# Optimization experiments

Measured on AMD Instinct MI355X. Metric: run time of the kernel, lower is better.

The kernel has to match this reference:

```python
import jax, jax.numpy as jnp
import numpy as np

N, E, D = 50000, 1200000, 64
NEG_SLOPE = 0.2  # PyG GATConv LeakyReLU slope
EPS_SM = 1e-16   # PyG softmax eps
EPS_LN = 1e-5


def _glorot(key, shape):
    fan = shape[0]
    return jax.random.normal(key, shape, jnp.float32) / np.float32(np.sqrt(fan))


def setup_inputs() -> dict:
    key = jax.random.key(0)
    ks = jax.random.split(key, 16)
    inp = {
        "x": jax.random.normal(ks[0], (N, D), jnp.float32),
        "edge_index": jax.random.randint(ks[1], (2, E), 0, N, dtype=jnp.int32),
        # layer 0: bipartite-style (-1,-1) GATConv -> separate src/dst projections
        "W_src0": _glorot(ks[2], (D, D)), "W_dst0": _glorot(ks[3], (D, D)),
        "a_src0": _glorot(ks[4], (D,)), "a_dst0": _glorot(ks[5], (D,)),
        "b0": jnp.zeros((D,), jnp.float32),
        "lin_W0": _glorot(ks[6], (D, D)), "lin_b0": jnp.zeros((D,), jnp.float32),
        # layers 1,2: int in_channels -> shared projection for src and dst
        "W1": _glorot(ks[7], (D, D)),
        "a_src1": _glorot(ks[8], (D,)), "a_dst1": _glorot(ks[9], (D,)),
        "b1": jnp.zeros((D,), jnp.float32),
        "lin_W1": _glorot(ks[10], (D, D)), "lin_b1": jnp.zeros((D,), jnp.float32),
        "W2": _glorot(ks[11], (D, D)),
        "a_src2": _glorot(ks[12], (D,)), "a_dst2": _glorot(ks[13], (D,)),
        "b2": jnp.zeros((D,), jnp.float32),
        "lin_W2": _glorot(ks[14], (D, D)), "lin_b2": jnp.zeros((D,), jnp.float32),
        "ln_w": jnp.ones((D,), jnp.float32), "ln_b": jnp.zeros((D,), jnp.float32),
        "proj_W": _glorot(ks[15], (D, 1)), "proj_b": jnp.zeros((1,), jnp.float32),
    }
    return inp


def _gat(x_src, x_dst, a_src, a_dst, bias, src, dst):
    # per-edge attention logit: a_src.x_j + a_dst.x_i, LeakyReLU
    alpha = (x_src * a_src).sum(-1)[src] + (x_dst * a_dst).sum(-1)[dst]  # [E]
    alpha = jnp.where(alpha >= 0, alpha, NEG_SLOPE * alpha)
    # segment softmax over edges sharing a destination node
    m = jax.ops.segment_max(alpha, dst, num_segments=N)
    m = jnp.where(jnp.isfinite(m), m, 0.0)  # empty segments -> -inf -> 0
    e = jnp.exp(alpha - m[dst])
    denom = jax.ops.segment_sum(e, dst, num_segments=N)
    w = e / (denom[dst] + EPS_SM)
    # weighted scatter-add aggregation
    return jax.ops.segment_sum(w[:, None] * x_src[src], dst, num_segments=N) + bias


def reference(x, edge_index,
              W_src0, W_dst0, a_src0, a_dst0, b0, lin_W0, lin_b0,
              W1, a_src1, a_dst1, b1, lin_W1, lin_b1,
              W2, a_src2, a_dst2, b2, lin_W2, lin_b2,
              ln_w, ln_b, proj_W, proj_b):
    src, dst = edge_index[0], edge_index[1]
    h = _gat(x @ W_src0, x @ W_dst0, a_src0, a_dst0, b0, src, dst) + x @ lin_W0 + lin_b0
    h = jax.nn.relu(h)
    hp = h @ W1
    h = _gat(hp, hp, a_src1, a_dst1, b1, src, dst) + h @ lin_W1 + lin_b1
    h = jax.nn.relu(h)
    hp = h @ W2
    h = _gat(hp, hp, a_src2, a_dst2, b2, src, dst) + h @ lin_W2 + lin_b2
    # PyG LayerNorm mode='graph': normalize over all nodes and channels
    mu = h.mean()
    var = h.var()
    h = (h - mu) * jax.lax.rsqrt(var + EPS_LN) * ln_w + ln_b
    return h @ proj_W + proj_b  # [N, 1]
```

## Files before the change

kernel.cpp:

```cpp
#include <hip/hip_runtime.h>
#include <hip/hip_bf16.h>

#define NN 50000
#define NE 1200000
#define D 64
#define NEG_SLOPE 0.2f
#define EPS_SM 1e-16f
#define EPS_LN 1e-5f
#define KMAX 4
#define BSH 6
#define NBUK 782
#define BCAP 2048
#define BCAPSH 11
#define EPB 4096
#define NPB 293
#define GP_NODES 32
#define GP_BLOCKS 1563
#define GAT_BLOCKS 12500

__device__ __forceinline__ float waveReduceSum(float v) {
    #pragma unroll
    for (int off = 32; off > 0; off >>= 1)
        v += __shfl_xor(v, off, 64);
    return v;
}
__device__ __forceinline__ float waveReduceMax(float v) {
    #pragma unroll
    for (int off = 32; off > 0; off >>= 1)
        v = fmaxf(v, __shfl_xor(v, off, 64));
    return v;
}
__device__ __forceinline__ float bflo(unsigned v) { return __uint_as_float(v << 16); }
__device__ __forceinline__ float bfhi(unsigned v) { return __uint_as_float(v & 0xffff0000u); }

template <bool HASD>
__global__ __launch_bounds__(256) void gemm_proj(
                          const float* __restrict__ hin,
                          const float* __restrict__ Wsrc,
                          const float* __restrict__ Wdst,
                          const float* __restrict__ Wlin,
                          const float* __restrict__ avs,
                          const float* __restrict__ avd,
                          const float* __restrict__ bgat,
                          const float* __restrict__ blin,
                          __hip_bfloat16* __restrict__ hp,
                          float* __restrict__ agg,
                          float* __restrict__ alpha_s,
                          float* __restrict__ alpha_d) {
    __shared__ float xt[GP_NODES * D];
    const int t   = threadIdx.x;
    const int nb0 = blockIdx.x * GP_NODES;
    const float4* src4 = (const float4*)(hin + (size_t)nb0 * D);
    float4* dst4 = (float4*)xt;
    if (nb0 + GP_NODES <= NN) {
        dst4[t]       = src4[t];
        dst4[t + 256] = src4[t + 256];
    } else {
        #pragma unroll
        for (int i = 0; i < 2; ++i) {
            const int idx = t + 256 * i;
            const int node = nb0 + (idx >> 4);
            dst4[idx] = (node < NN) ? src4[idx] : make_float4(0.f, 0.f, 0.f, 0.f);
        }
    }
    __syncthreads();

    const int wv   = t >> 6;
    const int lane = t & 63;
    const float* xw = xt + wv * 8 * D;

    float accs[8], accl[8], accd[HASD ? 8 : 1];
    #pragma unroll
    for (int m = 0; m < 8; ++m) { accs[m] = 0.f; accl[m] = 0.f; }
    if (HASD) {
        #pragma unroll
        for (int m = 0; m < 8; ++m) accd[m] = 0.f;
    }

    #pragma unroll 4
    for (int k = 0; k < D; k += 4) {
        float ws[4], wl[4], wd[4];
        #pragma unroll
        for (int j = 0; j < 4; ++j) {
            ws[j] = Wsrc[(k + j) * D + lane];
            wl[j] = Wlin[(k + j) * D + lane];
            if (HASD) wd[j] = Wdst[(k + j) * D + lane];
        }
        #pragma unroll
        for (int m = 0; m < 8; ++m) {
            const float4 xm = *(const float4*)(xw + m * D + k);
            accs[m] = fmaf(xm.x, ws[0], accs[m]);
            accs[m] = fmaf(xm.y, ws[1], accs[m]);
            accs[m] = fmaf(xm.z, ws[2], accs[m]);
            accs[m] = fmaf(xm.w, ws[3], accs[m]);
            accl[m] = fmaf(xm.x, wl[0], accl[m]);
            accl[m] = fmaf(xm.y, wl[1], accl[m]);
            accl[m] = fmaf(xm.z, wl[2], accl[m]);
            accl[m] = fmaf(xm.w, wl[3], accl[m]);
            if (HASD) {
                accd[m] = fmaf(xm.x, wd[0], accd[m]);
                accd[m] = fmaf(xm.y, wd[1], accd[m]);
                accd[m] = fmaf(xm.z, wd[2], accd[m]);
                accd[m] = fmaf(xm.w, wd[3], accd[m]);
            }
        }
    }

    const float avs_l = avs[lane], avd_l = avd[lane];
    const float bias  = blin[lane] + bgat[lane];
    #pragma unroll
    for (int m = 0; m < 8; ++m) {
        const int node = nb0 + wv * 8 + m;
        const float vs = waveReduceSum(accs[m] * avs_l);
        const float vd = waveReduceSum((HASD ? accd[m] : accs[m]) * avd_l);
        if (node < NN) {
            hp[(size_t)node * D + lane]  = __float2bfloat16(accs[m]);
            agg[(size_t)node * D + lane] = accl[m] + bias;
            if (lane == 0) {
                alpha_s[node] = vs;
                alpha_d[node] = vd;
            }
        }
    }
}

__global__ __launch_bounds__(256) void bucket_partition(const int* __restrict__ ei,
                                                        int* __restrict__ bcur,
                                                        int2* __restrict__ pairs) {
    __shared__ int h[NBUK];
    __shared__ int cur[NBUK];
    for (int i = threadIdx.x; i < NBUK; i += 256) h[i] = 0;
    __syncthreads();
    const int base = blockIdx.x * EPB;
    const int lim  = min(EPB, NE - base);
    for (int i = threadIdx.x; i < lim; i += 256)
        atomicAdd(&h[ei[NE + base + i] >> BSH], 1);
    __syncthreads();
    for (int i = threadIdx.x; i < NBUK; i += 256) {
        const int c = h[i];
        cur[i] = c ? atomicAdd(&bcur[i], c) : 0;
    }
    __syncthreads();
    for (int i = threadIdx.x; i < lim; i += 256) {
        const int s = ei[base + i];
        const int d = ei[NE + base + i];
        const int b = d >> BSH;
        const int pos = atomicAdd(&cur[b], 1);
        if (pos < BCAP) pairs[(b << BCAPSH) + pos] = make_int2(s, d);
    }
}

__global__ __launch_bounds__(256) void csr_finalize(const int2* __restrict__ pairs,
                                                    const int* __restrict__ bcur,
                                                    int* __restrict__ cnt,
                                                    int* __restrict__ row_start,
                                                    int* __restrict__ csr_src) {
    __shared__ int ncnt[64];
    __shared__ int lsrc[BCAP];
    const int t = threadIdx.x;
    const int b = blockIdx.x;
    const int beg = b << BCAPSH;
    const int m = min(bcur[b], BCAP);
    const int nbase = b << BSH;
    if (t < 64) ncnt[t] = 0;
    __syncthreads();
    for (int i = t; i < m; i += 256)
        atomicAdd(&ncnt[pairs[beg + i].y - nbase], 1);
    __syncthreads();
    if (t < 64) {
        const int v = ncnt[t];
        int inc = v;
        #pragma unroll
        for (int off = 1; off < 64; off <<= 1) {
            const int u = __shfl_up(inc, off, 64);
            if (t >= off) inc += u;
        }
        const int excl = inc - v;
        if (nbase + t < NN) {
            cnt[nbase + t] = v;
            row_start[nbase + t] = beg + excl;
        }
        ncnt[t] = excl;
    }
    __syncthreads();
    for (int i = t; i < m; i += 256) {
        const int2 p = pairs[beg + i];
        const int pos = atomicAdd(&ncnt[p.y - nbase], 1);
        lsrc[pos] = p.x;
    }
    __syncthreads();
    for (int i = t; i < m; i += 256)
        csr_src[beg + i] = lsrc[i];
}

template <bool DO_RELU, bool DO_STATS>
__global__ __launch_bounds__(256) void gat_node(
                         const int* __restrict__ csr_src,
                         const int* __restrict__ row_start,
                         const int* __restrict__ cnt,
                         const float* __restrict__ as,
                         const float* __restrict__ ad,
                         const __hip_bfloat16* __restrict__ hp,
                         float* __restrict__ agg,
                         float* __restrict__ partial) {
    __shared__ int2 esm[4][KMAX * 64];
    const int wv   = threadIdx.x >> 6;
    const int lane = threadIdx.x & 63;
    const int node = blockIdx.x * 4 + wv;
    const int snode = __builtin_amdgcn_readfirstlane(node);
    const int deg = cnt[snode];
    const int rs  = row_start[snode];
    const int half = lane >> 5;
    const int c2   = lane & 31;
    float2 acc = make_float2(0.f, 0.f);
    if (deg > 0) {
        const float ad_d = ad[snode];
        int   sr[KMAX];
        float ea[KMAX];
        float mx = -INFINITY;
        #pragma unroll
        for (int k = 0; k < KMAX; ++k) {
            const int j = k * 64 + lane;
            const bool valid = j < deg;
            const int s = valid ? csr_src[rs + j] : 0;
            float a = valid ? (as[s] + ad_d) : -INFINITY;
            a = (a >= 0.f) ? a : NEG_SLOPE * a;
            sr[k] = s;
            ea[k] = a;
            mx = fmaxf(mx, a);
        }
        mx = waveReduceMax(mx);
        float sum = 0.f;
        #pragma unroll
        for (int k = 0; k < KMAX; ++k) {
            float e = __expf(ea[k] - mx);
            e = (k * 64 + lane < deg) ? e : 0.f;
            ea[k] = e;
            sum += e;
        }
        sum = waveReduceSum(sum);
        const float inv = 1.f / (sum + EPS_SM);
        #pragma unroll
        for (int k = 0; k < KMAX; ++k) {
            if (k * 64 < deg)
                esm[wv][k * 64 + lane] = make_int2(sr[k] * 32, __float_as_int(ea[k] * inv));
        }
        const unsigned* hp32 = (const unsigned*)hp;
        const int jmax = (deg + 1) & ~1;
        float2 a0 = make_float2(0.f, 0.f), a1 = make_float2(0.f, 0.f);
        int j = 0;
        for (; j + 16 <= jmax; j += 16) {
            int2 p[8];
            unsigned v[8];
            #pragma unroll
            for (int u = 0; u < 8; ++u) p[u] = esm[wv][j + 2 * u + half];
            #pragma unroll
            for (int u = 0; u < 8; ++u) v[u] = hp32[p[u].x + c2];
            #pragma unroll
            for (int u = 0; u < 8; ++u) {
                const float w = __int_as_float(p[u].y);
                if (u & 1) {
                    a1.x = fmaf(w, bflo(v[u]), a1.x);
                    a1.y = fmaf(w, bfhi(v[u]), a1.y);
                } else {
                    a0.x = fmaf(w, bflo(v[u]), a0.x);
                    a0.y = fmaf(w, bfhi(v[u]), a0.y);
                }
            }
        }
        for (; j + 4 <= jmax; j += 4) {
            const int2 p0 = esm[wv][j + 0 + half];
            const int2 p1 = esm[wv][j + 2 + half];
            const unsigned v0 = hp32[p0.x + c2];
            const unsigned v1 = hp32[p1.x + c2];
            const float w0 = __int_as_float(p0.y), w1 = __int_as_float(p1.y);
            a0.x = fmaf(w0, bflo(v0), a0.x);
            a0.y = fmaf(w0, bfhi(v0), a0.y);
            a1.x = fmaf(w1, bflo(v1), a1.x);
            a1.y = fmaf(w1, bfhi(v1), a1.y);
        }
        for (; j < jmax; j += 2) {
            const int2 p = esm[wv][j + half];
            const unsigned v = hp32[p.x + c2];
            const float w = __int_as_float(p.y);
            a0.x = fmaf(w, bflo(v), a0.x);
            a0.y = fmaf(w, bfhi(v), a0.y);
        }
        acc.x = a0.x + a1.x;
        acc.y = a0.y + a1.y;
    }
    acc.x += __shfl_xor(acc.x, 32, 64);
    acc.y += __shfl_xor(acc.y, 32, 64);

    float2 r2 = make_float2(0.f, 0.f);
    if (half == 0) {
        const float2 g = *(const float2*)(agg + (size_t)node * D + 2 * c2);
        r2.x = g.x + acc.x;
        r2.y = g.y + acc.y;
        if (DO_RELU) { r2.x = fmaxf(r2.x, 0.f); r2.y = fmaxf(r2.y, 0.f); }
        *(float2*)(agg + (size_t)node * D + 2 * c2) = r2;
    }
    if (DO_STATS) {
        float s  = r2.x + r2.y;
        float ss = r2.x * r2.x + r2.y * r2.y;
        s  = waveReduceSum(s);
        ss = waveReduceSum(ss);
        __shared__ float red[2][4];
        if (lane == 0) { red[0][wv] = s; red[1][wv] = ss; }
        __syncthreads();
        if (threadIdx.x == 0) {
            partial[blockIdx.x]              = red[0][0] + red[0][1] + red[0][2] + red[0][3];
            partial[GAT_BLOCKS + blockIdx.x] = red[1][0] + red[1][1] + red[1][2] + red[1][3];
        }
    }
}

__global__ void ln_reduce(const float* __restrict__ partial, float* __restrict__ stats) {
    float s = 0.f, ss = 0.f;
    for (int i = threadIdx.x; i < GAT_BLOCKS; i += 256) {
        s  += partial[i];
        ss += partial[GAT_BLOCKS + i];
    }
    s  = waveReduceSum(s);
    ss = waveReduceSum(ss);
    __shared__ float sm[2][4];
    if ((threadIdx.x & 63) == 0) {
        sm[0][threadIdx.x >> 6] = s;
        sm[1][threadIdx.x >> 6] = ss;
    }
    __syncthreads();
    if (threadIdx.x == 0) {
        stats[0] = sm[0][0] + sm[0][1] + sm[0][2] + sm[0][3];
        stats[1] = sm[1][0] + sm[1][1] + sm[1][2] + sm[1][3];
    }
}

__global__ void finalize(const float* __restrict__ x,
                         const float* __restrict__ stats,
                         const float* __restrict__ lnw,
                         const float* __restrict__ lnb,
                         const float* __restrict__ pw,
                         const float* __restrict__ pb,
                         float* __restrict__ out) {
    const int wave = (blockIdx.x * blockDim.x + threadIdx.x) >> 6;
    const int lane = threadIdx.x & 63;
    if (wave >= NN) return;
    const float inv_nd = 1.f / (float)(NN * D);
    const float mu  = stats[0] * inv_nd;
    const float var = stats[1] * inv_nd - mu * mu;
    const float rs = rsqrtf(var + EPS_LN);
    const float v = x[(size_t)wave * D + lane];
    const float xn = (v - mu) * rs * lnw[lane] + lnb[lane];
    const float c = waveReduceSum(xn * pw[lane]);
    if (lane == 0) out[wave] = c + pb[0];
}

extern "C" void kernel_launch(void* const* d_in, const int* in_sizes, int n_in,
                              void* d_out, int out_size, void* d_ws, size_t ws_size,
                              hipStream_t stream) {
    const float* x     = (const float*)d_in[0];
    const int*   ei    = (const int*)d_in[1];
    const float* Wsrc0 = (const float*)d_in[2];
    const float* Wdst0 = (const float*)d_in[3];
    const float* asrc0 = (const float*)d_in[4];
    const float* adst0 = (const float*)d_in[5];
    const float* b0    = (const float*)d_in[6];
    const float* linW0 = (const float*)d_in[7];
    const float* linb0 = (const float*)d_in[8];
    const float* W1    = (const float*)d_in[9];
    const float* asrc1 = (const float*)d_in[10];
    const float* adst1 = (const float*)d_in[11];
    const float* b1    = (const float*)d_in[12];
    const float* linW1 = (const float*)d_in[13];
    const float* linb1 = (const float*)d_in[14];
    const float* W2    = (const float*)d_in[15];
    const float* asrc2 = (const float*)d_in[16];
    const float* adst2 = (const float*)d_in[17];
    const float* b2    = (const float*)d_in[18];
    const float* linW2 = (const float*)d_in[19];
    const float* linb2 = (const float*)d_in[20];
    const float* lnw   = (const float*)d_in[21];
    const float* lnb   = (const float*)d_in[22];
    const float* pW    = (const float*)d_in[23];
    const float* pb    = (const float*)d_in[24];
    float* out = (float*)d_out;

    int*  csr_src   = (int*)d_ws;
    int*  cnt       = csr_src + NBUK * BCAP;
    int*  row_start = cnt + NN;
    int*  bcur      = row_start + NN;
    size_t off = (size_t)(NBUK * BCAP + 2 * NN + NBUK);
    off = (off + 3) & ~(size_t)3;
    float* A     = (float*)d_ws + off;
    int2*  pairs = (int2*)A;
    float* B     = A + (size_t)NBUK * BCAP * 2;
    __hip_bfloat16* P = (__hip_bfloat16*)(B + NN * D);
    float* alpha_s = (float*)(P + NN * D);
    float* alpha_d = alpha_s + NN;
    float* stats   = alpha_d + NN;
    float* partial = stats + 2;

    const int elem_blocks = (NN * D) / 256;

    hipMemsetAsync(bcur, 0, NBUK * sizeof(int), stream);
    bucket_partition<<<NPB, 256, 0, stream>>>(ei, bcur, pairs);
    csr_finalize<<<NBUK, 256, 0, stream>>>(pairs, bcur, cnt, row_start, csr_src);

    gemm_proj<true><<<GP_BLOCKS, 256, 0, stream>>>(x, Wsrc0, Wdst0, linW0, asrc0, adst0,
                                                   b0, linb0, P, A, alpha_s, alpha_d);
    gat_node<true, false><<<GAT_BLOCKS, 256, 0, stream>>>(csr_src, row_start, cnt,
                                                          alpha_s, alpha_d, P, A, partial);

    gemm_proj<false><<<GP_BLOCKS, 256, 0, stream>>>(A, W1, W1, linW1, asrc1, adst1,
                                                    b1, linb1, P, B, alpha_s, alpha_d);
    gat_node<true, false><<<GAT_BLOCKS, 256, 0, stream>>>(csr_src, row_start, cnt,
                                                          alpha_s, alpha_d, P, B, partial);

    gemm_proj<false><<<GP_BLOCKS, 256, 0, stream>>>(B, W2, W2, linW2, asrc2, adst2,
                                                    b2, linb2, P, A, alpha_s, alpha_d);
    gat_node<false, true><<<GAT_BLOCKS, 256, 0, stream>>>(csr_src, row_start, cnt,
                                                          alpha_s, alpha_d, P, A, partial);

    ln_reduce<<<1, 256, 0, stream>>>(partial, stats);
    finalize<<<elem_blocks, 256, 0, stream>>>(A, stats, lnw, lnb, pW, pb, out);
}
```

Baseline: 362.8 us.

## Split GAT into softmax pass and channel-group-partitioned aggregation over feature slices

The fused per-node GAT kernel is split into a softmax kernel that writes normalized edge weights to a buffer, and an aggregation kernel launched four times as many blocks, each handling one 16-channel group. Projected features are stored in a group-major bf16 layout so each group's gather touches a 32-byte slice per source, with 8 edges processed per wave iteration. This aims to shrink the gathered working set per pass for better cache hit rates and more parallelism. In exchange it adds an extra kernel, a round trip of edge weights through memory, repeated CSR reads per group, and a much larger partial-sum array for the final reduction.

```diff
diff --git a/kernel.cpp b/kernel.cpp
--- a/kernel.cpp
+++ b/kernel.cpp
@@ -17,6 +17,8 @@
 #define GP_NODES 32
 #define GP_BLOCKS 1563
 #define GAT_BLOCKS 12500
+#define AGG_BLOCKS 50000
+#define NPART 50000
 
 __device__ __forceinline__ float waveReduceSum(float v) {
     #pragma unroll
@@ -43,7 +45,7 @@
                           const float* __restrict__ avd,
                           const float* __restrict__ bgat,
                           const float* __restrict__ blin,
-                          __hip_bfloat16* __restrict__ hp,
+                          unsigned* __restrict__ hpt,
                           float* __restrict__ agg,
                           float* __restrict__ alpha_s,
                           float* __restrict__ alpha_d) {
@@ -108,13 +110,22 @@
 
     const float avs_l = avs[lane], avd_l = avd[lane];
     const float bias  = blin[lane] + bgat[lane];
+    const int grp = lane >> 4;
+    const int cwi = (lane & 15) >> 1;
     #pragma unroll
     for (int m = 0; m < 8; ++m) {
         const int node = nb0 + wv * 8 + m;
         const float vs = waveReduceSum(accs[m] * avs_l);
         const float vd = waveReduceSum((HASD ? accd[m] : accs[m]) * avd_l);
+        __hip_bfloat16 hb = __float2bfloat16(accs[m]);
+        unsigned short raw;
+        __builtin_memcpy(&raw, &hb, 2);
+        const unsigned nbr = (unsigned)__shfl_down((int)raw, 1, 64) & 0xffffu;
         if (node < NN) {
-            hp[(size_t)node * D + lane]  = __float2bfloat16(accs[m]);
+            if (!(lane & 1)) {
+                const unsigned packed = (unsigned)raw | (nbr << 16);
+                hpt[(size_t)grp * (NN * 8) + (size_t)node * 8 + cwi] = packed;
+            }
             agg[(size_t)node * D + lane] = accl[m] + bias;
             if (lane == 0) {
                 alpha_s[node] = vs;
@@ -193,95 +204,100 @@
         csr_src[beg + i] = lsrc[i];
 }
 
-template <bool DO_RELU, bool DO_STATS>
-__global__ __launch_bounds__(256) void gat_node(
+__global__ __launch_bounds__(256) void gat_softmax(
                          const int* __restrict__ csr_src,
                          const int* __restrict__ row_start,
                          const int* __restrict__ cnt,
                          const float* __restrict__ as,
                          const float* __restrict__ ad,
-                         const __hip_bfloat16* __restrict__ hp,
-                         float* __restrict__ agg,
-                         float* __restrict__ partial) {
-    __shared__ int2 esm[4][KMAX * 64];
+                         float* __restrict__ wbuf) {
     const int wv   = threadIdx.x >> 6;
     const int lane = threadIdx.x & 63;
     const int node = blockIdx.x * 4 + wv;
     const int snode = __builtin_amdgcn_readfirstlane(node);
     const int deg = cnt[snode];
+    if (deg <= 0) return;
     const int rs  = row_start[snode];
-    const int half = lane >> 5;
-    const int c2   = lane & 31;
+    const float ad_d = ad[snode];
+    float ea[KMAX];
+    float mx = -INFINITY;
+    #pragma unroll
+    for (int k = 0; k < KMAX; ++k) {
+        const int j = k * 64 + lane;
+        const bool valid = j < deg;
+        const int s = valid ? csr_src[rs + j] : 0;
+        float a = valid ? (as[s] + ad_d) : -INFINITY;
+        a = (a >= 0.f) ? a : NEG_SLOPE * a;
+        ea[k] = a;
+        mx = fmaxf(mx, a);
+    }
+    mx = waveReduceMax(mx);
+    float sum = 0.f;
+    #pragma unroll
+    for (int k = 0; k < KMAX; ++k) {
+        float e = __expf(ea[k] - mx);
+        e = (k * 64 + lane < deg) ? e : 0.f;
+        ea[k] = e;
+        sum += e;
+    }
+    sum = waveReduceSum(sum);
+    const float inv = 1.f / (sum + EPS_SM);
+    #pragma unroll
+    for (int k = 0; k < KMAX; ++k) {
+        const int j = k * 64 + lane;
+        if (j < deg) wbuf[rs + j] = ea[k] * inv;
+    }
+}
+
+template <bool DO_RELU, bool DO_STATS>
+__global__ __launch_bounds__(256) void gat_agg(
+                         const int* __restrict__ csr_src,
+                         const int* __restrict__ row_start,
+                         const int* __restrict__ cnt,
+                         const float* __restrict__ wbuf,
+                         const unsigned* __restrict__ hpt,
+                         float* __restrict__ agg,
+                         float* __restrict__ partial) {
+    __shared__ int2 esm[4][KMAX * 64];
+    const int wv    = threadIdx.x >> 6;
+    const int lane  = threadIdx.x & 63;
+    const int group = blockIdx.x & 3;
+    const int node  = (blockIdx.x >> 2) * 4 + wv;
+    const int snode = __builtin_amdgcn_readfirstlane(node);
+    const int deg = cnt[snode];
+    const int rs  = row_start[snode];
+    const unsigned* gbase = hpt + (size_t)(blockIdx.x & 3) * (NN * 8);
     float2 acc = make_float2(0.f, 0.f);
     if (deg > 0) {
-        const float ad_d = ad[snode];
-        int   sr[KMAX];
-        float ea[KMAX];
-        float mx = -INFINITY;
         #pragma unroll
         for (int k = 0; k < KMAX; ++k) {
-            const int j = k * 64 + lane;
-            const bool valid = j < deg;
-            const int s = valid ? csr_src[rs + j] : 0;
-            float a = valid ? (as[s] + ad_d) : -INFINITY;
-            a = (a >= 0.f) ? a : NEG_SLOPE * a;
-            sr[k] = s;
-            ea[k] = a;
-            mx = fmaxf(mx, a);
-        }
-        mx = waveReduceMax(mx);
-        float sum = 0.f;
-        #pragma unroll
-        for (int k = 0; k < KMAX; ++k) {
-            float e = __expf(ea[k] - mx);
-            e = (k * 64 + lane < deg) ? e : 0.f;
-            ea[k] = e;
-            sum += e;
-        }
-        sum = waveReduceSum(sum);
-        const float inv = 1.f / (sum + EPS_SM);
-        #pragma unroll
-        for (int k = 0; k < KMAX; ++k) {
-            if (k * 64 < deg)
-                esm[wv][k * 64 + lane] = make_int2(sr[k] * 32, __float_as_int(ea[k] * inv));
-        }
-        const unsigned* hp32 = (const unsigned*)hp;
-        const int jmax = (deg + 1) & ~1;
+            if (k * 64 < deg) {
+                const int j = k * 64 + lane;
+                const bool valid = j < deg;
+                const int   s = valid ? csr_src[rs + j] : 0;
+                const float w = valid ? wbuf[rs + j] : 0.f;
+                esm[wv][j] = make_int2(s * 8, __float_as_int(w));
+            }
+        }
+        const int es = lane >> 3;
+        const int u  = lane & 7;
+        const int jmax = (deg + 7) & ~7;
         float2 a0 = make_float2(0.f, 0.f), a1 = make_float2(0.f, 0.f);
         int j = 0;
         for (; j + 16 <= jmax; j += 16) {
-            int2 p[8];
-            unsigned v[8];
-            #pragma unroll
-            for (int u = 0; u < 8; ++u) p[u] = esm[wv][j + 2 * u + half];
-            #pragma unroll
-            for (int u = 0; u < 8; ++u) v[u] = hp32[p[u].x + c2];
-            #pragma unroll
-            for (int u = 0; u < 8; ++u) {
-                const float w = __int_as_float(p[u].y);
-                if (u & 1) {
-                    a1.x = fmaf(w, bflo(v[u]), a1.x);
-                    a1.y = fmaf(w, bfhi(v[u]), a1.y);
-                } else {
-                    a0.x = fmaf(w, bflo(v[u]), a0.x);
-                    a0.y = fmaf(w, bfhi(v[u]), a0.y);
-                }
-            }
-        }
-        for (; j + 4 <= jmax; j += 4) {
-            const int2 p0 = esm[wv][j + 0 + half];
-            const int2 p1 = esm[wv][j + 2 + half];
-            const unsigned v0 = hp32[p0.x + c2];
-            const unsigned v1 = hp32[p1.x + c2];
-            const float w0 = __int_as_float(p0.y), w1 = __int_as_float(p1.y);
-            a0.x = fmaf(w0, bflo(v0), a0.x);
-            a0.y = fmaf(w0, bfhi(v0), a0.y);
-            a1.x = fmaf(w1, bflo(v1), a1.x);
-            a1.y = fmaf(w1, bfhi(v1), a1.y);
-        }
-        for (; j < jmax; j += 2) {
-            const int2 p = esm[wv][j + half];
-            const unsigned v = hp32[p.x + c2];
+            const int2 pa = esm[wv][j + es];
+            const int2 pb = esm[wv][j + 8 + es];
+            const unsigned va = gbase[pa.x + u];
+            const unsigned vb = gbase[pb.x + u];
+            const float wa = __int_as_float(pa.y), wb = __int_as_float(pb.y);
+            a0.x = fmaf(wa, bflo(va), a0.x);
+            a0.y = fmaf(wa, bfhi(va), a0.y);
+            a1.x = fmaf(wb, bflo(vb), a1.x);
+            a1.y = fmaf(wb, bfhi(vb), a1.y);
+        }
+        for (; j < jmax; j += 8) {
+            const int2 p = esm[wv][j + es];
+            const unsigned v = gbase[p.x + u];
             const float w = __int_as_float(p.y);
             a0.x = fmaf(w, bflo(v), a0.x);
             a0.y = fmaf(w, bfhi(v), a0.y);
@@ -289,16 +305,19 @@
         acc.x = a0.x + a1.x;
         acc.y = a0.y + a1.y;
     }
-    acc.x += __shfl_xor(acc.x, 32, 64);
-    acc.y += __shfl_xor(acc.y, 32, 64);
-
+    #pragma unroll
+    for (int off = 8; off <= 32; off <<= 1) {
+        acc.x += __shfl_xor(acc.x, off, 64);
+        acc.y += __shfl_xor(acc.y, off, 64);
+    }
     float2 r2 = make_float2(0.f, 0.f);
-    if (half == 0) {
-        const float2 g = *(const float2*)(agg + (size_t)node * D + 2 * c2);
+    if (lane < 8) {
+        float* ap = agg + (size_t)node * D + group * 16 + lane * 2;
+        const float2 g = *(const float2*)ap;
         r2.x = g.x + acc.x;
         r2.y = g.y + acc.y;
         if (DO_RELU) { r2.x = fmaxf(r2.x, 0.f); r2.y = fmaxf(r2.y, 0.f); }
-        *(float2*)(agg + (size_t)node * D + 2 * c2) = r2;
+        *(float2*)ap = r2;
     }
     if (DO_STATS) {
         float s  = r2.x + r2.y;
@@ -309,17 +328,17 @@
         if (lane == 0) { red[0][wv] = s; red[1][wv] = ss; }
         __syncthreads();
         if (threadIdx.x == 0) {
-            partial[blockIdx.x]              = red[0][0] + red[0][1] + red[0][2] + red[0][3];
-            partial[GAT_BLOCKS + blockIdx.x] = red[1][0] + red[1][1] + red[1][2] + red[1][3];
+            partial[blockIdx.x]         = red[0][0] + red[0][1] + red[0][2] + red[0][3];
+            partial[NPART + blockIdx.x] = red[1][0] + red[1][1] + red[1][2] + red[1][3];
         }
     }
 }
 
 __global__ void ln_reduce(const float* __restrict__ partial, float* __restrict__ stats) {
     float s = 0.f, ss = 0.f;
-    for (int i = threadIdx.x; i < GAT_BLOCKS; i += 256) {
+    for (int i = threadIdx.x; i < NPART; i += 256) {
         s  += partial[i];
-        ss += partial[GAT_BLOCKS + i];
+        ss += partial[NPART + i];
     }
     s  = waveReduceSum(s);
     ss = waveReduceSum(ss);
@@ -385,17 +404,18 @@
     const float* pb    = (const float*)d_in[24];
     float* out = (float*)d_out;
 
-    int*  csr_src   = (int*)d_ws;
-    int*  cnt       = csr_src + NBUK * BCAP;
-    int*  row_start = cnt + NN;
-    int*  bcur      = row_start + NN;
-    size_t off = (size_t)(NBUK * BCAP + 2 * NN + NBUK);
+    int*   csr_src   = (int*)d_ws;
+    float* wbuf      = (float*)(csr_src + NBUK * BCAP);
+    int*   cnt       = (int*)(wbuf + NBUK * BCAP);
+    int*   row_start = cnt + NN;
+    int*   bcur      = row_start + NN;
+    size_t off = (size_t)(2 * NBUK * BCAP + 2 * NN + NBUK);
     off = (off + 3) & ~(size_t)3;
     float* A     = (float*)d_ws + off;
     int2*  pairs = (int2*)A;
     float* B     = A + (size_t)NBUK * BCAP * 2;
-    __hip_bfloat16* P = (__hip_bfloat16*)(B + NN * D);
-    float* alpha_s = (float*)(P + NN * D);
+    unsigned* hpt = (unsigned*)(B + NN * D);
+    float* alpha_s = (float*)(hpt + (size_t)NN * D / 2);
     float* alpha_d = alpha_s + NN;
     float* stats   = alpha_d + NN;
     float* partial = stats + 2;
@@ -407,19 +427,22 @@
     csr_finalize<<<NBUK, 256, 0, stream>>>(pairs, bcur, cnt, row_start, csr_src);
 
     gemm_proj<true><<<GP_BLOCKS, 256, 0, stream>>>(x, Wsrc0, Wdst0, linW0, asrc0, adst0,
-                                                   b0, linb0, P, A, alpha_s, alpha_d);
-    gat_node<true, false><<<GAT_BLOCKS, 256, 0, stream>>>(csr_src, row_start, cnt,
-                                                          alpha_s, alpha_d, P, A, partial);
+                                                   b0, linb0, hpt, A, alpha_s, alpha_d);
+    gat_softmax<<<GAT_BLOCKS, 256, 0, stream>>>(csr_src, row_start, cnt, alpha_s, alpha_d, wbuf);
+    gat_agg<true, false><<<AGG_BLOCKS, 256, 0, stream>>>(csr_src, row_start, cnt,
+                                                         wbuf, hpt, A, partial);
 
     gemm_proj<false><<<GP_BLOCKS, 256, 0, stream>>>(A, W1, W1, linW1, asrc1, adst1,
-                                                    b1, linb1, P, B, alpha_s, alpha_d);
-    gat_node<true, false><<<GAT_BLOCKS, 256, 0, stream>>>(csr_src, row_start, cnt,
-                                                          alpha_s, alpha_d, P, B, partial);
+                                                    b1, linb1, hpt, B, alpha_s, alpha_d);
+    gat_softmax<<<GAT_BLOCKS, 256, 0, stream>>>(csr_src, row_start, cnt, alpha_s, alpha_d, wbuf);
+    gat_agg<true, false><<<AGG_BLOCKS, 256, 0, stream>>>(csr_src, row_start, cnt,
+                                                         wbuf, hpt, B, partial);
 
     gemm_proj<false><<<GP_BLOCKS, 256, 0, stream>>>(B, W2, W2, linW2, asrc2, adst2,
-                                                    b2, linb2, P, A, alpha_s, alpha_d);
-    gat_node<false, true><<<GAT_BLOCKS, 256, 0, stream>>>(csr_src, row_start, cnt,
-                                                          alpha_s, alpha_d, P, A, partial);
+                                                    b2, linb2, hpt, A, alpha_s, alpha_d);
+    gat_softmax<<<GAT_BLOCKS, 256, 0, stream>>>(csr_src, row_start, cnt, alpha_s, alpha_d, wbuf);
+    gat_agg<false, true><<<AGG_BLOCKS, 256, 0, stream>>>(csr_src, row_start, cnt,
+                                                         wbuf, hpt, A, partial);
 
     ln_reduce<<<1, 256, 0, stream>>>(partial, stats);
     finalize<<<elem_blocks, 256, 0, stream>>>(A, stats, lnw, lnb, pW, pb, out);
```

Result: slower. 536.7 us (+47.9%).

## Replace scalar FMA projection GEMMs with bf16 MFMA kernel and packed weights

Applied to the files above, without the earlier changes.

Replaces the per-layer FP32 FMA projection kernel with an MFMA-based kernel (16x16x32 bf16) that handles 16 nodes per block. Weights are first packed into bf16 MFMA operand layout by a new pack_w kernel, and the attention logits are reduced through shuffles plus shared memory. The inputs to the linear/residual path are now rounded to bf16, which lowers precision of the agg output. Separately, the 16-wide unrolled gather loop in the GAT aggregation is removed, leaving the 4-wide loop.

```diff
diff --git a/kernel.cpp b/kernel.cpp
--- a/kernel.cpp
+++ b/kernel.cpp
@@ -14,9 +14,11 @@
 #define BCAPSH 11
 #define EPB 4096
 #define NPB 293
-#define GP_NODES 32
-#define GP_BLOCKS 1563
+#define GEMM_BLOCKS 3125
 #define GAT_BLOCKS 12500
+
+typedef __attribute__((ext_vector_type(8))) short short8;
+typedef __attribute__((ext_vector_type(4))) float float4v;
 
 __device__ __forceinline__ float waveReduceSum(float v) {
     #pragma unroll
@@ -32,13 +34,35 @@
 }
 __device__ __forceinline__ float bflo(unsigned v) { return __uint_as_float(v << 16); }
 __device__ __forceinline__ float bfhi(unsigned v) { return __uint_as_float(v & 0xffff0000u); }
-
-template <bool HASD>
-__global__ __launch_bounds__(256) void gemm_proj(
+__device__ __forceinline__ short f2bf_bits(float f) {
+    __hip_bfloat16 b = __float2bfloat16(f);
+    short v; __builtin_memcpy(&v, &b, 2);
+    return v;
+}
+
+__global__ void pack_w(const float* __restrict__ W0,
+                       const float* __restrict__ W1m,
+                       const float* __restrict__ W2m,
+                       unsigned short* __restrict__ wpk, int nmats) {
+    const int n = nmats * 4096;
+    for (int idx = blockIdx.x * 256 + threadIdx.x; idx < n; idx += gridDim.x * 256) {
+        const int j = idx & 7;
+        const int lane = (idx >> 3) & 63;
+        const int khtile = idx >> 9;
+        const int kh = khtile & 1;
+        const int tile = khtile >> 1;
+        const int mat = tile >> 2;
+        const int ch = (tile & 3) * 16 + (lane & 15);
+        const int k = kh * 32 + (lane >> 4) * 8 + j;
+        const float* W = (mat == 0) ? W0 : (mat == 1 ? W1m : W2m);
+        wpk[idx] = (unsigned short)f2bf_bits(W[k * D + ch]);
+    }
+}
+
+template <int NMATS>
+__global__ __launch_bounds__(256) void gemm_mfma(
                           const float* __restrict__ hin,
-                          const float* __restrict__ Wsrc,
-                          const float* __restrict__ Wdst,
-                          const float* __restrict__ Wlin,
+                          const unsigned short* __restrict__ wpk,
                           const float* __restrict__ avs,
                           const float* __restrict__ avd,
                           const float* __restrict__ bgat,
@@ -47,80 +71,88 @@
                           float* __restrict__ agg,
                           float* __restrict__ alpha_s,
                           float* __restrict__ alpha_d) {
-    __shared__ float xt[GP_NODES * D];
+    constexpr int NT   = NMATS * 4;
+    constexpr int NTPW = NT / 4;
+    __shared__ float xt[16 * D];
+    __shared__ float ared[2][4][16];
+
     const int t   = threadIdx.x;
-    const int nb0 = blockIdx.x * GP_NODES;
-    const float4* src4 = (const float4*)(hin + (size_t)nb0 * D);
-    float4* dst4 = (float4*)xt;
-    if (nb0 + GP_NODES <= NN) {
-        dst4[t]       = src4[t];
-        dst4[t + 256] = src4[t + 256];
-    } else {
-        #pragma unroll
-        for (int i = 0; i < 2; ++i) {
-            const int idx = t + 256 * i;
-            const int node = nb0 + (idx >> 4);
-            dst4[idx] = (node < NN) ? src4[idx] : make_float4(0.f, 0.f, 0.f, 0.f);
-        }
-    }
-    __syncthreads();
-
-    const int wv   = t >> 6;
+    const int nb0 = blockIdx.x * 16;
+    ((float4*)xt)[t] = ((const float4*)(hin + (size_t)nb0 * D))[t];
+    __syncthreads();
+
+    const int w    = t >> 6;
     const int lane = t & 63;
-    const float* xw = xt + wv * 8 * D;
-
-    float accs[8], accl[8], accd[HASD ? 8 : 1];
-    #pragma unroll
-    for (int m = 0; m < 8; ++m) { accs[m] = 0.f; accl[m] = 0.f; }
-    if (HASD) {
-        #pragma unroll
-        for (int m = 0; m < 8; ++m) accd[m] = 0.f;
-    }
-
-    #pragma unroll 4
-    for (int k = 0; k < D; k += 4) {
-        float ws[4], wl[4], wd[4];
-        #pragma unroll
-        for (int j = 0; j < 4; ++j) {
-            ws[j] = Wsrc[(k + j) * D + lane];
-            wl[j] = Wlin[(k + j) * D + lane];
-            if (HASD) wd[j] = Wdst[(k + j) * D + lane];
-        }
-        #pragma unroll
-        for (int m = 0; m < 8; ++m) {
-            const float4 xm = *(const float4*)(xw + m * D + k);
-            accs[m] = fmaf(xm.x, ws[0], accs[m]);
-            accs[m] = fmaf(xm.y, ws[1], accs[m]);
-            accs[m] = fmaf(xm.z, ws[2], accs[m]);
-            accs[m] = fmaf(xm.w, ws[3], accs[m]);
-            accl[m] = fmaf(xm.x, wl[0], accl[m]);
-            accl[m] = fmaf(xm.y, wl[1], accl[m]);
-            accl[m] = fmaf(xm.z, wl[2], accl[m]);
-            accl[m] = fmaf(xm.w, wl[3], accl[m]);
-            if (HASD) {
-                accd[m] = fmaf(xm.x, wd[0], accd[m]);
-                accd[m] = fmaf(xm.y, wd[1], accd[m]);
-                accd[m] = fmaf(xm.z, wd[2], accd[m]);
-                accd[m] = fmaf(xm.w, wd[3], accd[m]);
+    const int mrow = lane & 15;
+    const int kq   = lane >> 4;
+
+    short8 a[2];
+    #pragma unroll
+    for (int kh = 0; kh < 2; ++kh) {
+        const float* xp = xt + mrow * D + kh * 32 + kq * 8;
+        const float4 f0 = *(const float4*)(xp);
+        const float4 f1 = *(const float4*)(xp + 4);
+        a[kh][0] = f2bf_bits(f0.x); a[kh][1] = f2bf_bits(f0.y);
+        a[kh][2] = f2bf_bits(f0.z); a[kh][3] = f2bf_bits(f0.w);
+        a[kh][4] = f2bf_bits(f1.x); a[kh][5] = f2bf_bits(f1.y);
+        a[kh][6] = f2bf_bits(f1.z); a[kh][7] = f2bf_bits(f1.w);
+    }
+
+    float4v acc[NTPW];
+    #pragma unroll
+    for (int i = 0; i < NTPW; ++i) {
+        const int tile = w * NTPW + i;
+        const short8 b0 = *(const short8*)(wpk + ((size_t)(tile * 2 + 0) * 64 + lane) * 8);
+        const short8 b1 = *(const short8*)(wpk + ((size_t)(tile * 2 + 1) * 64 + lane) * 8);
+        float4v c = {0.f, 0.f, 0.f, 0.f};
+        c = __builtin_amdgcn_mfma_f32_16x16x32_bf16(a[0], b0, c, 0, 0, 0);
+        c = __builtin_amdgcn_mfma_f32_16x16x32_bf16(a[1], b1, c, 0, 0, 0);
+        acc[i] = c;
+    }
+
+    float psr[4] = {0.f, 0.f, 0.f, 0.f};
+    float pdr[4] = {0.f, 0.f, 0.f, 0.f};
+    #pragma unroll
+    for (int i = 0; i < NTPW; ++i) {
+        const int tile = w * NTPW + i;
+        const int mat  = tile >> 2;
+        const int c64  = (tile & 3) * 16 + mrow;
+        const float av_s = avs[c64], av_d = avd[c64];
+        const float bias = blin[c64] + bgat[c64];
+        #pragma unroll
+        for (int r = 0; r < 4; ++r) {
+            const int node = nb0 + kq * 4 + r;
+            const float v = acc[i][r];
+            if (mat == 0) {
+                hp[(size_t)node * D + c64] = __float2bfloat16(v);
+                psr[r] += v * av_s;
+                if (NMATS == 2) pdr[r] += v * av_d;
+            } else if (NMATS == 3 && mat == 1) {
+                pdr[r] += v * av_d;
+            } else {
+                agg[(size_t)node * D + c64] = v + bias;
             }
         }
     }
-
-    const float avs_l = avs[lane], avd_l = avd[lane];
-    const float bias  = blin[lane] + bgat[lane];
-    #pragma unroll
-    for (int m = 0; m < 8; ++m) {
-        const int node = nb0 + wv * 8 + m;
-        const float vs = waveReduceSum(accs[m] * avs_l);
-        const float vd = waveReduceSum((HASD ? accd[m] : accs[m]) * avd_l);
-        if (node < NN) {
-            hp[(size_t)node * D + lane]  = __float2bfloat16(accs[m]);
-            agg[(size_t)node * D + lane] = accl[m] + bias;
-            if (lane == 0) {
-                alpha_s[node] = vs;
-                alpha_d[node] = vd;
-            }
-        }
+    #pragma unroll
+    for (int off = 1; off < 16; off <<= 1) {
+        #pragma unroll
+        for (int r = 0; r < 4; ++r) {
+            psr[r] += __shfl_xor(psr[r], off, 64);
+            pdr[r] += __shfl_xor(pdr[r], off, 64);
+        }
+    }
+    if (mrow == 0) {
+        #pragma unroll
+        for (int r = 0; r < 4; ++r) {
+            ared[0][w][kq * 4 + r] = psr[r];
+            ared[1][w][kq * 4 + r] = pdr[r];
+        }
+    }
+    __syncthreads();
+    if (t < 16) {
+        alpha_s[nb0 + t] = ared[0][0][t] + ared[0][1][t] + ared[0][2][t] + ared[0][3][t];
+        alpha_d[nb0 + t] = ared[1][0][t] + ared[1][1][t] + ared[1][2][t] + ared[1][3][t];
     }
 }
 
@@ -249,25 +281,6 @@
         const int jmax = (deg + 1) & ~1;
         float2 a0 = make_float2(0.f, 0.f), a1 = make_float2(0.f, 0.f);
         int j = 0;
-        for (; j + 16 <= jmax; j += 16) {
-            int2 p[8];
-            unsigned v[8];
-            #pragma unroll
-            for (int u = 0; u < 8; ++u) p[u] = esm[wv][j + 2 * u + half];
-            #pragma unroll
-            for (int u = 0; u < 8; ++u) v[u] = hp32[p[u].x + c2];
-            #pragma unroll
-            for (int u = 0; u < 8; ++u) {
-                const float w = __int_as_float(p[u].y);
-                if (u & 1) {
-                    a1.x = fmaf(w, bflo(v[u]), a1.x);
-                    a1.y = fmaf(w, bfhi(v[u]), a1.y);
-                } else {
-                    a0.x = fmaf(w, bflo(v[u]), a0.x);
-                    a0.y = fmaf(w, bfhi(v[u]), a0.y);
-                }
-            }
-        }
         for (; j + 4 <= jmax; j += 4) {
             const int2 p0 = esm[wv][j + 0 + half];
             const int2 p1 = esm[wv][j + 2 + half];
@@ -399,6 +412,7 @@
     float* alpha_d = alpha_s + NN;
     float* stats   = alpha_d + NN;
     float* partial = stats + 2;
+    unsigned short* wpk = (unsigned short*)(((uintptr_t)(partial + 2 * GAT_BLOCKS) + 15) & ~(uintptr_t)15);
 
     const int elem_blocks = (NN * D) / 256;
 
@@ -406,18 +420,21 @@
     bucket_partition<<<NPB, 256, 0, stream>>>(ei, bcur, pairs);
     csr_finalize<<<NBUK, 256, 0, stream>>>(pairs, bcur, cnt, row_start, csr_src);
 
-    gemm_proj<true><<<GP_BLOCKS, 256, 0, stream>>>(x, Wsrc0, Wdst0, linW0, asrc0, adst0,
-                                                   b0, linb0, P, A, alpha_s, alpha_d);
+    pack_w<<<48, 256, 0, stream>>>(Wsrc0, Wdst0, linW0, wpk, 3);
+    gemm_mfma<3><<<GEMM_BLOCKS, 256, 0, stream>>>(x, wpk, asrc0, adst0, b0, linb0,
+                                                  P, A, alpha_s, alpha_d);
     gat_node<true, false><<<GAT_BLOCKS, 256, 0, stream>>>(csr_src, row_start, cnt,
                                                           alpha_s, alpha_d, P, A, partial);
 
-    gemm_proj<false><<<GP_BLOCKS, 256, 0, stream>>>(A, W1, W1, linW1, asrc1, adst1,
-                                                    b1, linb1, P, B, alpha_s, alpha_d);
+    pack_w<<<32, 256, 0, stream>>>(W1, linW1, linW1, wpk, 2);
+    gemm_mfma<2><<<GEMM_BLOCKS, 256, 0, stream>>>(A, wpk, asrc1, adst1, b1, linb1,
+                                                  P, B, alpha_s, alpha_d);
     gat_node<true, false><<<GAT_BLOCKS, 256, 0, stream>>>(csr_src, row_start, cnt,
                                                           alpha_s, alpha_d, P, B, partial);
 
-    gemm_proj<false><<<GP_BLOCKS, 256, 0, stream>>>(B, W2, W2, linW2, asrc2, adst2,
-                                                    b2, linb2, P, A, alpha_s, alpha_d);
+    pack_w<<<32, 256, 0, stream>>>(W2, linW2, linW2, wpk, 2);
+    gemm_mfma<2><<<GEMM_BLOCKS, 256, 0, stream>>>(B, wpk, asrc2, adst2, b2, linb2,
+                                                  P, A, alpha_s, alpha_d);
     gat_node<false, true><<<GAT_BLOCKS, 256, 0, stream>>>(csr_src, row_start, cnt,
                                                           alpha_s, alpha_d, P, A, partial);
 
```

Result: faster. 338.6 us (-6.7%).
